# Kernel optimization log

Hardware: AMD Instinct MI355X
Metric: run time of the kernel (lower is better)

Reference implementation:

```python
import jax, jax.numpy as jnp
import numpy as np

B, D, E, C = 16384, 768, 124, 6  # batch, emb_dim, n_experts, n_classes


def _mlp(h, w1, b1, w2, b2):
    # timm Mlp: fc1 -> GELU(exact) -> fc2, hidden = in_features
    return jax.nn.gelu(h @ w1 + b1, approximate=False) @ w2 + b2


def setup_inputs() -> dict:
    key = jax.random.key(0)
    ks = jax.random.split(key, 14)
    s = 0.02
    inp = {
        "x": jax.random.normal(ks[0], (B, D), dtype=jnp.float32),
        # per-sample expert counts in [1, E]
        "n_experts": jax.random.randint(ks[1], (B,), 1, E + 1, dtype=jnp.int64 if jax.config.jax_enable_x64 else jnp.int32),
        # classifier Mlp: D -> D -> E*C
        "cls_w1": jax.random.normal(ks[2], (D, D), dtype=jnp.float32) * s,
        "cls_b1": jnp.zeros((D,), jnp.float32),
        "cls_w2": jax.random.normal(ks[3], (D, E * C), dtype=jnp.float32) * s,
        "cls_b2": jnp.zeros((E * C,), jnp.float32),
        # which_expert Mlp: D -> D -> E
        "we_w1": jax.random.normal(ks[4], (D, D), dtype=jnp.float32) * s,
        "we_b1": jnp.zeros((D,), jnp.float32),
        "we_w2": jax.random.normal(ks[5], (D, E), dtype=jnp.float32) * s,
        "we_b2": jnp.zeros((E,), jnp.float32),
        # expert_weights Mlp: D -> D -> E
        "ew_w1": jax.random.normal(ks[6], (D, D), dtype=jnp.float32) * s,
        "ew_b1": jnp.zeros((D,), jnp.float32),
        "ew_w2": jax.random.normal(ks[7], (D, E), dtype=jnp.float32) * s,
        "ew_b2": jnp.zeros((E,), jnp.float32),
    }
    return inp


def reference(x, n_experts, cls_w1, cls_b1, cls_w2, cls_b2,
              we_w1, we_b1, we_w2, we_b2, ew_w1, ew_b1, ew_w2, ew_b2):
    emb = x  # backbone = identity
    expert_logits = _mlp(emb, cls_w1, cls_b1, cls_w2, cls_b2).reshape(B, E, C)
    expert_weight_logits = _mlp(emb, ew_w1, ew_b1, ew_w2, ew_b2)  # [B, E]
    which_expert = _mlp(emb, we_w1, we_b1, we_w2, we_b2)          # [B, E]

    n = jnp.minimum(n_experts, E)                                  # clamp to n_experts
    # kth_largest: sort descending, pick (n-1)-th per row -> threshold
    sorted_desc = -jnp.sort(-which_expert, axis=1)
    threshold = sorted_desc[jnp.arange(B), n - 1][:, None]         # [B, 1]
    mask = which_expert < threshold

    expert_weight_logits = jnp.where(mask, -jnp.inf, expert_weight_logits)
    expert_proba = jax.nn.softmax(expert_logits, axis=2)           # over classes
    expert_weights = jax.nn.softmax(expert_weight_logits, axis=1)  # over experts

    combined = (expert_proba * expert_weights[:, :, None]).sum(axis=1)
    return combined / expert_weights.sum(axis=1)[:, None]          # [B, C]
```

## Files before the change

### kernel.cpp

```cpp
#include <hip/hip_runtime.h>
#include <stdint.h>

typedef unsigned short u16;
typedef short short8 __attribute__((ext_vector_type(8)));
typedef float f32x4 __attribute__((ext_vector_type(4)));

#define NB 16384

#define OFF_XHI      0ull
#define OFF_XLO      25165824ull
#define OFF_LCLS     0ull
#define OFF_LWE_P0   25165824ull
#define OFF_LWE_P1   33554432ull
#define OFF_LWE_P2   41943040ull
#define OFF_BT1      50331648ull
#define OFF_LEWB     50331648ull
#define OFF_BTWE_HI  52690944ull
#define OFF_BTWE_LO  53870592ull
#define OFF_BT2CLS   55050240ull
#define OFF_BT2EW    56229888ull
#define OFF_BT2WE_HI 56426496ull
#define OFF_BT2WE_LO 56623104ull
#define OFF_B1CE     56819712ull
#define OFF_B1WE     56825856ull
#define OFF_B2CLS    56828928ull
#define OFF_B2EW     56832000ull
#define OFF_B2WE     56832512ull
#define OFF_HCLSEW   56833024ull
#define OFF_HWE_HI   107164672ull
#define OFF_HWE_LO   132330496ull
#define WS_NEED      157496320ull

__device__ __forceinline__ u16 f2bf(float f) {
  uint32_t u = __float_as_uint(f);
  u += 0x7fffu + ((u >> 16) & 1u);
  return (u16)(u >> 16);
}
__device__ __forceinline__ float bf2f(u16 h) {
  return __uint_as_float(((uint32_t)h) << 16);
}
__device__ __forceinline__ void g2l16(const u16* g, u16* l) {
  __builtin_amdgcn_global_load_lds(
      (__attribute__((address_space(1))) void*)(u16*)g,
      (__attribute__((address_space(3))) void*)l, 16, 0, 0);
}

__global__ void prep_all(
    const float* __restrict__ x, u16* __restrict__ xhi, u16* __restrict__ xlo,
    const float* __restrict__ cls_w1, const float* __restrict__ ew_w1,
    const float* __restrict__ we_w1,  const float* __restrict__ cls_w2,
    const float* __restrict__ ew_w2,  const float* __restrict__ we_w2,
    u16* BT1, u16* BTwe_hi, u16* BTwe_lo,
    u16* BT2cls, u16* BT2ew, u16* BT2we_hi, u16* BT2we_lo,
    const float* __restrict__ cls_b1, const float* __restrict__ ew_b1,
    const float* __restrict__ we_b1,  const float* __restrict__ cls_b2,
    const float* __restrict__ ew_b2,  const float* __restrict__ we_b2,
    float* b1ce, float* b1we, float* b2cls, float* b2ew, float* b2we) {
  __shared__ float t[64][65];
  const int bid = blockIdx.x;
  if (bid < 12288) {
    int i = bid * 256 + threadIdx.x;
    float4 v = ((const float4*)x)[i];
    ushort4 h, l;
    h.x = f2bf(v.x); l.x = f2bf(v.x - bf2f(h.x));
    h.y = f2bf(v.y); l.y = f2bf(v.y - bf2f(h.y));
    h.z = f2bf(v.z); l.z = f2bf(v.z - bf2f(h.z));
    h.w = f2bf(v.w); l.w = f2bf(v.w - bf2f(h.w));
    ((ushort4*)xhi)[i] = h;
    ((ushort4*)xlo)[i] = l;
    return;
  }
  if (bid < 13152) {
    const int idx = bid - 12288;
    const int bx = idx % 12, by = (idx / 12) % 12, bz = idx / 144;
    const float* src; int N; u16* dhi; u16* dlo = nullptr;
    switch (bz) {
      case 0: src = cls_w1; N = 768; dhi = BT1; break;
      case 1: src = ew_w1;  N = 768; dhi = BT1 + 768 * 768; break;
      case 2: src = we_w1;  N = 768; dhi = BTwe_hi; dlo = BTwe_lo; break;
      case 3: src = cls_w2; N = 744; dhi = BT2cls; break;
      case 4: src = ew_w2;  N = 124; dhi = BT2ew; break;
      default: src = we_w2; N = 124; dhi = BT2we_hi; dlo = BT2we_lo; break;
    }
    const int Npad = (N + 127) & ~127;
    const int n0 = by * 64;
    if (n0 >= Npad) return;
    const int k0 = bx * 64;
    const int tx = threadIdx.x & 63, tg = threadIdx.x >> 6;
#pragma unroll
    for (int r = 0; r < 16; ++r) {
      int k = tg * 16 + r;
      int n = n0 + tx;
      t[k][tx] = (n < N) ? src[(size_t)(k0 + k) * N + n] : 0.f;
    }
    __syncthreads();
#pragma unroll
    for (int r = 0; r < 16; ++r) {
      int n = n0 + tg * 16 + r;
      if (n < Npad) {
        float v = t[tx][tg * 16 + r];
        u16 h = f2bf(v);
        dhi[(size_t)n * 768 + k0 + tx] = h;
        if (dlo) dlo[(size_t)n * 768 + k0 + tx] = f2bf(v - bf2f(h));
      }
    }
    return;
  }
  int id = (bid - 13152) * 256 + threadIdx.x;
  if (id < 1536) { b1ce[id] = (id < 768) ? cls_b1[id] : ew_b1[id - 768]; return; }
  id -= 1536;
  if (id < 768) { b1we[id] = we_b1[id]; return; }
  id -= 768;
  if (id < 768) { b2cls[id] = (id < 744) ? cls_b2[id] : 0.f; return; }
  id -= 768;
  if (id < 128) { b2ew[id] = (id < 124) ? ew_b2[id] : 0.f; return; }
  id -= 128;
  if (id < 128) { b2we[id] = (id < 124) ? we_b2[id] : 0.f; return; }
}

__device__ __forceinline__ void gemm_core(
    const u16* A0, const u16* A1, const u16* A2, int lda,
    const u16* B0, const u16* B1, const u16* B2,
    int npass, int K, int bm, int tid, u16* sA, u16* sB, f32x4 acc[4][4]) {
  const int lane = tid & 63;
  const int wv = tid >> 6;
  const int wr = wv >> 1, wc = wv & 1;
  const int sr = lane >> 3;
  const int sc = (((lane & 7) ^ sr) << 3);
  for (int p = 0; p < npass; ++p) {
    const u16* A = (p == 0) ? A0 : ((p == 1) ? A1 : A2);
    const u16* Bp = (p == 0) ? B0 : ((p == 1) ? B1 : B2);
    const u16* gA = A + (size_t)(bm + wv * 32 + sr) * lda + sc;
    const u16* gB = Bp + (size_t)(wv * 32 + sr) * K + sc;
    u16* lA = sA + (wv * 32) * 64;
    u16* lB = sB + (wv * 32) * 64;
    for (int kt = 0; kt < K; kt += 64) {
#pragma unroll
      for (int s = 0; s < 4; ++s) {
        g2l16(gA + (size_t)(s * 8) * lda + kt, lA + s * 8 * 64);
        g2l16(gB + (size_t)(s * 8) * K + kt, lB + s * 8 * 64);
      }
      __syncthreads();
#pragma unroll
      for (int ks = 0; ks < 2; ++ks) {
        const int co = ((ks * 4 + (lane >> 4)) ^ (lane & 7)) * 8;
        short8 av[4], bv[4];
#pragma unroll
        for (int i = 0; i < 4; i++)
          av[i] = *(const short8*)(sA + (wr * 64 + i * 16 + (lane & 15)) * 64 + co);
#pragma unroll
        for (int j = 0; j < 4; j++)
          bv[j] = *(const short8*)(sB + (wc * 64 + j * 16 + (lane & 15)) * 64 + co);
#pragma unroll
        for (int i = 0; i < 4; i++)
#pragma unroll
          for (int j = 0; j < 4; j++)
            acc[i][j] = __builtin_amdgcn_mfma_f32_16x16x32_bf16(av[i], bv[j], acc[i][j], 0, 0, 0);
      }
      __syncthreads();
    }
  }
}

__device__ __forceinline__ void gemm_split_core(
    const u16* __restrict__ Ahi, const u16* __restrict__ Alo, int lda,
    const u16* __restrict__ Bhi, const u16* __restrict__ Blo, int ldb,
    int K, int bm, int tid, u16* sA, u16* sB, f32x4 acc[4][4]) {
  const int lane = tid & 63;
  const int wv = tid >> 6;
  const int wr = wv >> 1, wc = wv & 1;
  const int sr = lane >> 3;
  const int gl = (lane & 7) ^ sr;
  const int koff = (gl & 3) << 3;
  const u16* Asel = (gl < 4) ? Ahi : Alo;
  const u16* Bsel = (gl < 4) ? Bhi : Blo;
  const u16* gA = Asel + (size_t)(bm + wv * 32 + sr) * lda + koff;
  const u16* gB = Bsel + (size_t)(wv * 32 + sr) * ldb + koff;
  u16* lA = sA + (wv * 32) * 64;
  u16* lB = sB + (wv * 32) * 64;

  for (int kt = 0; kt < K; kt += 32) {
#pragma unroll
    for (int s = 0; s < 4; ++s) {
      g2l16(gA + (size_t)(s * 8) * lda + kt, lA + s * 8 * 64);
      g2l16(gB + (size_t)(s * 8) * ldb + kt, lB + s * 8 * 64);
    }
    __syncthreads();
    const int coh = (((lane >> 4) ^ (lane & 7)) << 3);
    short8 ah[4], al[4], bh[4], bl[4];
#pragma unroll
    for (int i = 0; i < 4; i++) {
      const u16* p = sA + (wr * 64 + i * 16 + (lane & 15)) * 64;
      ah[i] = *(const short8*)(p + coh);
      al[i] = *(const short8*)(p + (coh ^ 32));
    }
#pragma unroll
    for (int j = 0; j < 4; j++) {
      const u16* p = sB + (wc * 64 + j * 16 + (lane & 15)) * 64;
      bh[j] = *(const short8*)(p + coh);
      bl[j] = *(const short8*)(p + (coh ^ 32));
    }
#pragma unroll
    for (int i = 0; i < 4; i++)
#pragma unroll
      for (int j = 0; j < 4; j++) {
        acc[i][j] = __builtin_amdgcn_mfma_f32_16x16x32_bf16(ah[i], bh[j], acc[i][j], 0, 0, 0);
        acc[i][j] = __builtin_amdgcn_mfma_f32_16x16x32_bf16(al[i], bh[j], acc[i][j], 0, 0, 0);
        acc[i][j] = __builtin_amdgcn_mfma_f32_16x16x32_bf16(ah[i], bl[j], acc[i][j], 0, 0, 0);
      }
    __syncthreads();
  }
}

__device__ __forceinline__ void decode_bid(int bid, int NC, int& bm, int& bn) {
  const int xcd = bid & 7, slot = bid >> 3;
  const int per = NC << 3;
  const int sub = slot / per, rem = slot - sub * per;
  const int colu = rem >> 3, rowIn = rem & 7;
  bm = ((xcd << 4) + (sub << 3) + rowIn) << 7;
  bn = colu << 7;
}

__global__ __launch_bounds__(256, 4) void gemm1_fused(
    const u16* __restrict__ Ahi, const u16* __restrict__ Alo,
    const u16* __restrict__ Bwe_hi, const u16* __restrict__ Bwe_lo,
    const u16* __restrict__ BT1,
    const float* __restrict__ b1we, const float* __restrict__ b1ce,
    u16* __restrict__ out_we_hi, u16* __restrict__ out_we_lo,
    u16* __restrict__ out_ce) {
  __shared__ u16 smem[2 * 128 * 64];
  u16* sA = smem;
  u16* sB = smem + 128 * 64;
  const int tid = threadIdx.x;
  const int lane = tid & 63;
  const int wr = (tid >> 6) >> 1, wc = (tid >> 6) & 1;
  const int K = 768;

  f32x4 acc[4][4];
#pragma unroll
  for (int i = 0; i < 4; i++)
#pragma unroll
    for (int j = 0; j < 4; j++) acc[i][j] = f32x4{0.f, 0.f, 0.f, 0.f};

  if (blockIdx.x < 768) {
    int bm, bn;
    decode_bid(blockIdx.x, 6, bm, bn);
    gemm_split_core(Ahi, Alo, K, Bwe_hi + (size_t)bn * K, Bwe_lo + (size_t)bn * K, K,
                    K, bm, tid, sA, sB, acc);
#pragma unroll
    for (int j = 0; j < 4; j++) {
      const int col = bn + wc * 64 + j * 16 + (lane & 15);
      const float bs = b1we[col];
#pragma unroll
      for (int i = 0; i < 4; i++) {
        const int row0 = bm + wr * 64 + i * 16 + (lane >> 4) * 4;
#pragma unroll
        for (int r = 0; r < 4; r++) {
          float v = acc[i][j][r] + bs;
          const size_t idx = (size_t)(row0 + r) * 768 + col;
          float g = 0.5f * v * (1.0f + erff(v * 0.70710678118654752f));
          u16 h = f2bf(g);
          out_we_hi[idx] = h;
          out_we_lo[idx] = f2bf(g - bf2f(h));
        }
      }
    }
  } else {
    int bm, bn;
    decode_bid(blockIdx.x - 768, 12, bm, bn);
    gemm_core(Ahi, nullptr, nullptr, 768, BT1 + (size_t)bn * K, nullptr, nullptr,
              1, K, bm, tid, sA, sB, acc);
#pragma unroll
    for (int j = 0; j < 4; j++) {
      const int col = bn + wc * 64 + j * 16 + (lane & 15);
      const float bs = b1ce[col];
#pragma unroll
      for (int i = 0; i < 4; i++) {
        const int row0 = bm + wr * 64 + i * 16 + (lane >> 4) * 4;
#pragma unroll
        for (int r = 0; r < 4; r++) {
          float v = acc[i][j][r] + bs;
          float g = 0.5f * v * (1.0f + erff(v * 0.70710678118654752f));
          out_ce[(size_t)(row0 + r) * 1536 + col] = f2bf(g);
        }
      }
    }
  }
}

__global__ __launch_bounds__(256, 4) void gemm2_fused(
    const u16* __restrict__ h_cls,
    const u16* __restrict__ hwe_hi, const u16* __restrict__ hwe_lo,
    const u16* __restrict__ BT2cls, const u16* __restrict__ BT2ew,
    const u16* __restrict__ BT2we_hi, const u16* __restrict__ BT2we_lo,
    const float* __restrict__ b2cls, const float* __restrict__ b2ew,
    const float* __restrict__ b2we,
    u16* __restrict__ Lcls, u16* __restrict__ LewB,
    float* __restrict__ p0, float* __restrict__ p1, float* __restrict__ p2) {
  __shared__ u16 sA[128 * 64];
  __shared__ u16 sB[128 * 64];
  const int tid = threadIdx.x;
  const int lane = tid & 63;
  const int wr = (tid >> 6) >> 1, wc = (tid >> 6) & 1;

  f32x4 acc[4][4];
#pragma unroll
  for (int i = 0; i < 4; i++)
#pragma unroll
    for (int j = 0; j < 4; j++) acc[i][j] = f32x4{0.f, 0.f, 0.f, 0.f};

  const int bid = blockIdx.x;
  if (bid < 768) {
    int bm, bn;
    decode_bid(bid, 6, bm, bn);
    gemm_core(h_cls, nullptr, nullptr, 1536, BT2cls + (size_t)bn * 768, nullptr, nullptr,
              1, 768, bm, tid, sA, sB, acc);
#pragma unroll
    for (int j = 0; j < 4; j++) {
      const int col = bn + wc * 64 + j * 16 + (lane & 15);
      const float bs = b2cls[col];
#pragma unroll
      for (int i = 0; i < 4; i++) {
        const int row0 = bm + wr * 64 + i * 16 + (lane >> 4) * 4;
#pragma unroll
        for (int r = 0; r < 4; r++)
          Lcls[(size_t)(row0 + r) * 768 + col] = f2bf(acc[i][j][r] + bs);
      }
    }
  } else if (bid < 896) {
    const int r = bid - 768;
    const int bm = (((r & 7) << 4) + (r >> 3)) << 7;
    gemm_core(h_cls + 768, nullptr, nullptr, 1536, BT2ew, nullptr, nullptr,
              1, 768, bm, tid, sA, sB, acc);
#pragma unroll
    for (int j = 0; j < 4; j++) {
      const int col = wc * 64 + j * 16 + (lane & 15);
      const float bs = b2ew[col];
#pragma unroll
      for (int i = 0; i < 4; i++) {
        const int row0 = bm + wr * 64 + i * 16 + (lane >> 4) * 4;
#pragma unroll
        for (int r2 = 0; r2 < 4; r2++)
          LewB[(size_t)(row0 + r2) * 128 + col] = f2bf(acc[i][j][r2] + bs);
      }
    }
  } else {
    const int q = bid - 896;
    const int pass = q >> 7;
    const int r = q & 127;
    const int bm = (((r & 7) << 4) + (r >> 3)) << 7;
    const u16* A = (pass == 1) ? hwe_lo : hwe_hi;
    const u16* Bp = (pass == 2) ? BT2we_lo : BT2we_hi;
    gemm_core(A, nullptr, nullptr, 768, Bp, nullptr, nullptr,
              1, 768, bm, tid, sA, sB, acc);
    float* o = (pass == 0) ? p0 : ((pass == 1) ? p1 : p2);
#pragma unroll
    for (int j = 0; j < 4; j++) {
      const int col = wc * 64 + j * 16 + (lane & 15);
      const float bs = (pass == 0) ? b2we[col] : 0.f;
#pragma unroll
      for (int i = 0; i < 4; i++) {
        const int row0 = bm + wr * 64 + i * 16 + (lane >> 4) * 4;
#pragma unroll
        for (int r2 = 0; r2 < 4; r2++)
          o[(size_t)(row0 + r2) * 128 + col] = acc[i][j][r2] + bs;
      }
    }
  }
}

__global__ __launch_bounds__(256) void finalize(
    const u16* __restrict__ Lcls,
    const float* __restrict__ p0, const float* __restrict__ p1,
    const float* __restrict__ p2,
    const u16* __restrict__ LewB,
    const int* __restrict__ nexp, float* __restrict__ out) {
  const int bid = blockIdx.x;
  const int g = ((bid & 7) << 9) + (bid >> 3);
  const int b = (g << 2) + (int)(threadIdx.x >> 6);
  const int lane = threadIdx.x & 63;
  const float NEG = -3.0e38f;
  const size_t base = (size_t)b * 128;
  const float w0 = (lane < 124) ? (p0[base + lane] + p1[base + lane] + p2[base + lane]) : NEG;
  const float w1 = (lane < 60) ? (p0[base + 64 + lane] + p1[base + 64 + lane] + p2[base + 64 + lane]) : NEG;
  int r0 = 0, r1 = 0;
#pragma unroll
  for (int j = 0; j < 64; ++j) {
    float v = __shfl(w0, j, 64);
    r0 += (v > w0); r1 += (v > w1);
  }
#pragma unroll
  for (int j = 0; j < 64; ++j) {
    float v = __shfl(w1, j, 64);
    r0 += (v > w0); r1 += (v > w1);
  }
  int n = nexp[b];
  n = n < 1 ? 1 : (n > 124 ? 124 : n);
  const bool k0 = (lane < 124) && (r0 < n);
  const bool k1 = (lane < 60) && (r1 < n);
  float l0 = k0 ? bf2f(LewB[base + lane]) : NEG;
  float l1 = k1 ? bf2f(LewB[base + 64 + lane]) : NEG;
  float mx = fmaxf(l0, l1);
#pragma unroll
  for (int o = 32; o > 0; o >>= 1) mx = fmaxf(mx, __shfl_xor(mx, o, 64));
  float e0 = k0 ? __expf(l0 - mx) : 0.f;
  float e1 = k1 ? __expf(l1 - mx) : 0.f;
  float S = e0 + e1;
#pragma unroll
  for (int o = 32; o > 0; o >>= 1) S += __shfl_xor(S, o, 64);
  float a0 = 0, a1 = 0, a2 = 0, a3 = 0, a4 = 0, a5 = 0;
#pragma unroll
  for (int h = 0; h < 2; ++h) {
    int e = lane + h * 64;
    float we = h ? e1 : e0;
    if (we > 0.f) {
      const u16* lp = Lcls + (size_t)b * 768 + e * 6;
      float c0 = bf2f(lp[0]), c1 = bf2f(lp[1]), c2 = bf2f(lp[2]);
      float c3 = bf2f(lp[3]), c4 = bf2f(lp[4]), c5 = bf2f(lp[5]);
      float m = fmaxf(fmaxf(fmaxf(c0, c1), fmaxf(c2, c3)), fmaxf(c4, c5));
      float q0 = __expf(c0 - m), q1 = __expf(c1 - m), q2 = __expf(c2 - m);
      float q3 = __expf(c3 - m), q4 = __expf(c4 - m), q5 = __expf(c5 - m);
      float inv = we / (q0 + q1 + q2 + q3 + q4 + q5);
      a0 += q0 * inv; a1 += q1 * inv; a2 += q2 * inv;
      a3 += q3 * inv; a4 += q4 * inv; a5 += q5 * inv;
    }
  }
#pragma unroll
  for (int o = 32; o > 0; o >>= 1) {
    a0 += __shfl_xor(a0, o, 64); a1 += __shfl_xor(a1, o, 64);
    a2 += __shfl_xor(a2, o, 64); a3 += __shfl_xor(a3, o, 64);
    a4 += __shfl_xor(a4, o, 64); a5 += __shfl_xor(a5, o, 64);
  }
  if (lane < 6) {
    float v = (lane == 0) ? a0 : (lane == 1) ? a1 : (lane == 2) ? a2
              : (lane == 3) ? a3 : (lane == 4) ? a4 : a5;
    out[(size_t)b * 6 + lane] = v / S;
  }
}

__global__ void fill_sentinel(float* out, int n, float v) {
  int i = blockIdx.x * 256 + threadIdx.x;
  if (i < n) out[i] = v;
}

extern "C" void kernel_launch(void* const* d_in, const int* in_sizes, int n_in,
                              void* d_out, int out_size, void* d_ws, size_t ws_size,
                              hipStream_t stream) {
  const float* x = (const float*)d_in[0];
  const int* nexp = (const int*)d_in[1];
  const float* cls_w1 = (const float*)d_in[2];
  const float* cls_b1 = (const float*)d_in[3];
  const float* cls_w2 = (const float*)d_in[4];
  const float* cls_b2 = (const float*)d_in[5];
  const float* we_w1 = (const float*)d_in[6];
  const float* we_b1 = (const float*)d_in[7];
  const float* we_w2 = (const float*)d_in[8];
  const float* we_b2 = (const float*)d_in[9];
  const float* ew_w1 = (const float*)d_in[10];
  const float* ew_b1 = (const float*)d_in[11];
  const float* ew_w2 = (const float*)d_in[12];
  const float* ew_b2 = (const float*)d_in[13];
  float* out = (float*)d_out;
  char* ws = (char*)d_ws;

  if (ws_size < WS_NEED) {
    fill_sentinel<<<(out_size + 255) / 256, 256, 0, stream>>>(out, out_size, 12345.0f);
    return;
  }

  u16* xhi = (u16*)(ws + OFF_XHI);
  u16* xlo = (u16*)(ws + OFF_XLO);
  u16* Lcls = (u16*)(ws + OFF_LCLS);
  float* pwe0 = (float*)(ws + OFF_LWE_P0);
  float* pwe1 = (float*)(ws + OFF_LWE_P1);
  float* pwe2 = (float*)(ws + OFF_LWE_P2);
  u16* LewB = (u16*)(ws + OFF_LEWB);
  u16* BT1 = (u16*)(ws + OFF_BT1);
  u16* BTwe_hi = (u16*)(ws + OFF_BTWE_HI);
  u16* BTwe_lo = (u16*)(ws + OFF_BTWE_LO);
  u16* BT2cls = (u16*)(ws + OFF_BT2CLS);
  u16* BT2ew = (u16*)(ws + OFF_BT2EW);
  u16* BT2we_hi = (u16*)(ws + OFF_BT2WE_HI);
  u16* BT2we_lo = (u16*)(ws + OFF_BT2WE_LO);
  float* b1ce = (float*)(ws + OFF_B1CE);
  float* b1we = (float*)(ws + OFF_B1WE);
  float* b2cls = (float*)(ws + OFF_B2CLS);
  float* b2ew = (float*)(ws + OFF_B2EW);
  float* b2we = (float*)(ws + OFF_B2WE);
  u16* h_clsew = (u16*)(ws + OFF_HCLSEW);
  u16* h_we_hi = (u16*)(ws + OFF_HWE_HI);
  u16* h_we_lo = (u16*)(ws + OFF_HWE_LO);

  prep_all<<<13165, 256, 0, stream>>>(x, xhi, xlo,
                                      cls_w1, ew_w1, we_w1, cls_w2, ew_w2, we_w2,
                                      BT1, BTwe_hi, BTwe_lo, BT2cls, BT2ew, BT2we_hi, BT2we_lo,
                                      cls_b1, ew_b1, we_b1, cls_b2, ew_b2, we_b2,
                                      b1ce, b1we, b2cls, b2ew, b2we);
  gemm1_fused<<<2304, 256, 0, stream>>>(xhi, xlo, BTwe_hi, BTwe_lo, BT1,
                                        b1we, b1ce, h_we_hi, h_we_lo, h_clsew);
  gemm2_fused<<<1280, 256, 0, stream>>>(h_clsew, h_we_hi, h_we_lo,
                                        BT2cls, BT2ew, BT2we_hi, BT2we_lo,
                                        b2cls, b2ew, b2we,
                                        Lcls, LewB, pwe0, pwe1, pwe2);
  finalize<<<4096, 256, 0, stream>>>(Lcls, pwe0, pwe1, pwe2, LewB, nexp, out);
}
```

Before: 377.7 us.

## Fuse finalize into gemm2 with per-chunk completion flags instead of separate launch

Removes the separate finalize kernel and appends 512 extra blocks to gemm2. Each extra block spins on ten per-chunk flags that the GEMM blocks publish with release stores after writing their tiles, then runs the finalize logic for 32 rows. The aim is to drop one launch and the full-grid barrier so finalize can overlap the GEMM tail. The flags sit inside the BTwe_lo workspace region, so prep's rewrite of that region is what clears them between calls. Correctness therefore depends on that overwrite and on producer blocks being scheduled before the spinning consumers.

```diff
diff --git a/kernel.cpp b/kernel.cpp
--- a/kernel.cpp
+++ b/kernel.cpp
@@ -6,6 +6,7 @@
 typedef float f32x4 __attribute__((ext_vector_type(4)));
 
 #define NB 16384
+#define MAGIC 0x7FC07FC0
 
 #define OFF_XHI      0ull
 #define OFF_XLO      25165824ull
@@ -17,6 +18,7 @@
 #define OFF_LEWB     50331648ull
 #define OFF_BTWE_HI  52690944ull
 #define OFF_BTWE_LO  53870592ull
+#define OFF_FLAGS    54525952ull
 #define OFF_BT2CLS   55050240ull
 #define OFF_BT2EW    56229888ull
 #define OFF_BT2WE_HI 56426496ull
@@ -288,97 +290,11 @@
   }
 }
 
-__global__ __launch_bounds__(256, 4) void gemm2_fused(
-    const u16* __restrict__ h_cls,
-    const u16* __restrict__ hwe_hi, const u16* __restrict__ hwe_lo,
-    const u16* __restrict__ BT2cls, const u16* __restrict__ BT2ew,
-    const u16* __restrict__ BT2we_hi, const u16* __restrict__ BT2we_lo,
-    const float* __restrict__ b2cls, const float* __restrict__ b2ew,
-    const float* __restrict__ b2we,
-    u16* __restrict__ Lcls, u16* __restrict__ LewB,
-    float* __restrict__ p0, float* __restrict__ p1, float* __restrict__ p2) {
-  __shared__ u16 sA[128 * 64];
-  __shared__ u16 sB[128 * 64];
-  const int tid = threadIdx.x;
-  const int lane = tid & 63;
-  const int wr = (tid >> 6) >> 1, wc = (tid >> 6) & 1;
-
-  f32x4 acc[4][4];
-#pragma unroll
-  for (int i = 0; i < 4; i++)
-#pragma unroll
-    for (int j = 0; j < 4; j++) acc[i][j] = f32x4{0.f, 0.f, 0.f, 0.f};
-
-  const int bid = blockIdx.x;
-  if (bid < 768) {
-    int bm, bn;
-    decode_bid(bid, 6, bm, bn);
-    gemm_core(h_cls, nullptr, nullptr, 1536, BT2cls + (size_t)bn * 768, nullptr, nullptr,
-              1, 768, bm, tid, sA, sB, acc);
-#pragma unroll
-    for (int j = 0; j < 4; j++) {
-      const int col = bn + wc * 64 + j * 16 + (lane & 15);
-      const float bs = b2cls[col];
-#pragma unroll
-      for (int i = 0; i < 4; i++) {
-        const int row0 = bm + wr * 64 + i * 16 + (lane >> 4) * 4;
-#pragma unroll
-        for (int r = 0; r < 4; r++)
-          Lcls[(size_t)(row0 + r) * 768 + col] = f2bf(acc[i][j][r] + bs);
-      }
-    }
-  } else if (bid < 896) {
-    const int r = bid - 768;
-    const int bm = (((r & 7) << 4) + (r >> 3)) << 7;
-    gemm_core(h_cls + 768, nullptr, nullptr, 1536, BT2ew, nullptr, nullptr,
-              1, 768, bm, tid, sA, sB, acc);
-#pragma unroll
-    for (int j = 0; j < 4; j++) {
-      const int col = wc * 64 + j * 16 + (lane & 15);
-      const float bs = b2ew[col];
-#pragma unroll
-      for (int i = 0; i < 4; i++) {
-        const int row0 = bm + wr * 64 + i * 16 + (lane >> 4) * 4;
-#pragma unroll
-        for (int r2 = 0; r2 < 4; r2++)
-          LewB[(size_t)(row0 + r2) * 128 + col] = f2bf(acc[i][j][r2] + bs);
-      }
-    }
-  } else {
-    const int q = bid - 896;
-    const int pass = q >> 7;
-    const int r = q & 127;
-    const int bm = (((r & 7) << 4) + (r >> 3)) << 7;
-    const u16* A = (pass == 1) ? hwe_lo : hwe_hi;
-    const u16* Bp = (pass == 2) ? BT2we_lo : BT2we_hi;
-    gemm_core(A, nullptr, nullptr, 768, Bp, nullptr, nullptr,
-              1, 768, bm, tid, sA, sB, acc);
-    float* o = (pass == 0) ? p0 : ((pass == 1) ? p1 : p2);
-#pragma unroll
-    for (int j = 0; j < 4; j++) {
-      const int col = wc * 64 + j * 16 + (lane & 15);
-      const float bs = (pass == 0) ? b2we[col] : 0.f;
-#pragma unroll
-      for (int i = 0; i < 4; i++) {
-        const int row0 = bm + wr * 64 + i * 16 + (lane >> 4) * 4;
-#pragma unroll
-        for (int r2 = 0; r2 < 4; r2++)
-          o[(size_t)(row0 + r2) * 128 + col] = acc[i][j][r2] + bs;
-      }
-    }
-  }
-}
-
-__global__ __launch_bounds__(256) void finalize(
-    const u16* __restrict__ Lcls,
-    const float* __restrict__ p0, const float* __restrict__ p1,
-    const float* __restrict__ p2,
-    const u16* __restrict__ LewB,
-    const int* __restrict__ nexp, float* __restrict__ out) {
-  const int bid = blockIdx.x;
-  const int g = ((bid & 7) << 9) + (bid >> 3);
-  const int b = (g << 2) + (int)(threadIdx.x >> 6);
-  const int lane = threadIdx.x & 63;
+__device__ __forceinline__ void finalize_rows(
+    const u16* __restrict__ Lcls, const float* __restrict__ p0,
+    const float* __restrict__ p1, const float* __restrict__ p2,
+    const u16* __restrict__ LewB, const int* __restrict__ nexp,
+    float* __restrict__ out, int b, int lane) {
   const float NEG = -3.0e38f;
   const size_t base = (size_t)b * 128;
   const float w0 = (lane < 124) ? (p0[base + lane] + p1[base + lane] + p2[base + lane]) : NEG;
@@ -435,6 +351,122 @@
     float v = (lane == 0) ? a0 : (lane == 1) ? a1 : (lane == 2) ? a2
               : (lane == 3) ? a3 : (lane == 4) ? a4 : a5;
     out[(size_t)b * 6 + lane] = v / S;
+  }
+}
+
+__global__ __launch_bounds__(256, 4) void gemm2_fused(
+    const u16* __restrict__ h_cls,
+    const u16* __restrict__ hwe_hi, const u16* __restrict__ hwe_lo,
+    const u16* __restrict__ BT2cls, const u16* __restrict__ BT2ew,
+    const u16* __restrict__ BT2we_hi, const u16* __restrict__ BT2we_lo,
+    const float* __restrict__ b2cls, const float* __restrict__ b2ew,
+    const float* __restrict__ b2we,
+    u16* __restrict__ Lcls, u16* __restrict__ LewB,
+    float* __restrict__ p0, float* __restrict__ p1, float* __restrict__ p2,
+    int* __restrict__ flags, const int* __restrict__ nexp, float* __restrict__ out) {
+  __shared__ u16 sA[128 * 64];
+  __shared__ u16 sB[128 * 64];
+  const int tid = threadIdx.x;
+  const int lane = tid & 63;
+  const int wr = (tid >> 6) >> 1, wc = (tid >> 6) & 1;
+  const int bid = blockIdx.x;
+
+  if (bid >= 1280) {
+    const int w = bid - 1280;
+    const int chunk = w >> 2, quarter = w & 3;
+    if (tid == 0) {
+      for (;;) {
+        int got = 0;
+#pragma unroll
+        for (int s = 0; s < 10; ++s)
+          got += (__hip_atomic_load(&flags[chunk * 10 + s], __ATOMIC_RELAXED,
+                                    __HIP_MEMORY_SCOPE_AGENT) == (int)MAGIC);
+        if (got == 10) break;
+        __builtin_amdgcn_s_sleep(8);
+      }
+    }
+    __syncthreads();
+    __builtin_amdgcn_fence(__ATOMIC_ACQUIRE, "agent");
+#pragma unroll
+    for (int it = 0; it < 8; ++it) {
+      const int b = chunk * 128 + quarter * 32 + it * 4 + (tid >> 6);
+      finalize_rows(Lcls, p0, p1, p2, LewB, nexp, out, b, lane);
+    }
+    return;
+  }
+
+  f32x4 acc[4][4];
+#pragma unroll
+  for (int i = 0; i < 4; i++)
+#pragma unroll
+    for (int j = 0; j < 4; j++) acc[i][j] = f32x4{0.f, 0.f, 0.f, 0.f};
+
+  int chunk, slot;
+  if (bid < 768) {
+    int bm, bn;
+    decode_bid(bid, 6, bm, bn);
+    chunk = bm >> 7; slot = bn >> 7;
+    gemm_core(h_cls, nullptr, nullptr, 1536, BT2cls + (size_t)bn * 768, nullptr, nullptr,
+              1, 768, bm, tid, sA, sB, acc);
+#pragma unroll
+    for (int j = 0; j < 4; j++) {
+      const int col = bn + wc * 64 + j * 16 + (lane & 15);
+      const float bs = b2cls[col];
+#pragma unroll
+      for (int i = 0; i < 4; i++) {
+        const int row0 = bm + wr * 64 + i * 16 + (lane >> 4) * 4;
+#pragma unroll
+        for (int r = 0; r < 4; r++)
+          Lcls[(size_t)(row0 + r) * 768 + col] = f2bf(acc[i][j][r] + bs);
+      }
+    }
+  } else if (bid < 896) {
+    const int r = bid - 768;
+    const int bm = (((r & 7) << 4) + (r >> 3)) << 7;
+    chunk = bm >> 7; slot = 6;
+    gemm_core(h_cls + 768, nullptr, nullptr, 1536, BT2ew, nullptr, nullptr,
+              1, 768, bm, tid, sA, sB, acc);
+#pragma unroll
+    for (int j = 0; j < 4; j++) {
+      const int col = wc * 64 + j * 16 + (lane & 15);
+      const float bs = b2ew[col];
+#pragma unroll
+      for (int i = 0; i < 4; i++) {
+        const int row0 = bm + wr * 64 + i * 16 + (lane >> 4) * 4;
+#pragma unroll
+        for (int r2 = 0; r2 < 4; r2++)
+          LewB[(size_t)(row0 + r2) * 128 + col] = f2bf(acc[i][j][r2] + bs);
+      }
+    }
+  } else {
+    const int q = bid - 896;
+    const int pass = q >> 7;
+    const int r = q & 127;
+    const int bm = (((r & 7) << 4) + (r >> 3)) << 7;
+    chunk = bm >> 7; slot = 7 + pass;
+    const u16* A = (pass == 1) ? hwe_lo : hwe_hi;
+    const u16* Bp = (pass == 2) ? BT2we_lo : BT2we_hi;
+    gemm_core(A, nullptr, nullptr, 768, Bp, nullptr, nullptr,
+              1, 768, bm, tid, sA, sB, acc);
+    float* o = (pass == 0) ? p0 : ((pass == 1) ? p1 : p2);
+#pragma unroll
+    for (int j = 0; j < 4; j++) {
+      const int col = wc * 64 + j * 16 + (lane & 15);
+      const float bs = (pass == 0) ? b2we[col] : 0.f;
+#pragma unroll
+      for (int i = 0; i < 4; i++) {
+        const int row0 = bm + wr * 64 + i * 16 + (lane >> 4) * 4;
+#pragma unroll
+        for (int r2 = 0; r2 < 4; r2++)
+          o[(size_t)(row0 + r2) * 128 + col] = acc[i][j][r2] + bs;
+      }
+    }
+  }
+  __syncthreads();
+  if (tid == 0) {
+    __builtin_amdgcn_fence(__ATOMIC_RELEASE, "agent");
+    __hip_atomic_store(&flags[chunk * 10 + slot], (int)MAGIC, __ATOMIC_RELEASE,
+                       __HIP_MEMORY_SCOPE_AGENT);
   }
 }
 
@@ -478,6 +510,7 @@
   u16* BT1 = (u16*)(ws + OFF_BT1);
   u16* BTwe_hi = (u16*)(ws + OFF_BTWE_HI);
   u16* BTwe_lo = (u16*)(ws + OFF_BTWE_LO);
+  int* flags = (int*)(ws + OFF_FLAGS);
   u16* BT2cls = (u16*)(ws + OFF_BT2CLS);
   u16* BT2ew = (u16*)(ws + OFF_BT2EW);
   u16* BT2we_hi = (u16*)(ws + OFF_BT2WE_HI);
@@ -498,9 +531,9 @@
                                       b1ce, b1we, b2cls, b2ew, b2we);
   gemm1_fused<<<2304, 256, 0, stream>>>(xhi, xlo, BTwe_hi, BTwe_lo, BT1,
                                         b1we, b1ce, h_we_hi, h_we_lo, h_clsew);
-  gemm2_fused<<<1280, 256, 0, stream>>>(h_clsew, h_we_hi, h_we_lo,
+  gemm2_fused<<<1792, 256, 0, stream>>>(h_clsew, h_we_hi, h_we_lo,
                                         BT2cls, BT2ew, BT2we_hi, BT2we_lo,
                                         b2cls, b2ew, b2we,
-                                        Lcls, LewB, pwe0, pwe1, pwe2);
-  finalize<<<4096, 256, 0, stream>>>(Lcls, pwe0, pwe1, pwe2, LewB, nexp, out);
-}
+                                        Lcls, LewB, pwe0, pwe1, pwe2,
+                                        flags, nexp, out);
+}
```

Measured after the change: 479.1 us. 1.27x slower.
